# Performance work log

Hardware: AMD Instinct MI355X
Metric: run time of the kernel (lower is better)

The kernel has to match this reference:

```python
import jax, jax.numpy as jnp
import numpy as np

N = 50000   # full-order mesh size
n = 10      # latent dim
MU = 32     # neighbourhood / window size
B = 8       # batch of snapshots


def setup_inputs() -> dict:
    key = jax.random.key(0)
    ks = jax.random.split(key, 6)
    x = jax.random.normal(ks[0], (B, N), jnp.float32)
    enc_w = jax.random.normal(ks[1], (n, N), jnp.float32) * 0.01  # torch Linear weight [n, N]
    enc_b = jax.random.normal(ks[2], (n,), jnp.float32) * 0.01
    decoder = jax.random.uniform(ks[3], (n, N), jnp.float32, minval=-0.01, maxval=0.01)
    bandwidth_layers = jax.random.uniform(ks[4], (n, n, N), jnp.float32, minval=-0.01, maxval=0.01)
    neighbours = jax.random.randint(ks[5], (N, MU), 0, N, jnp.int32)
    return dict(x=x, enc_w=enc_w, enc_b=enc_b, decoder=decoder,
                bandwidth_layers=bandwidth_layers, neighbours=neighbours)


def reference(x, enc_w, enc_b, decoder, bandwidth_layers, neighbours):
    mu = neighbours.shape[1]
    # encode: torch Linear -> x @ W.T + b                      [B, n]
    encoded = x @ enc_w.T + enc_b
    # bandwidths: bmm(encoded.repeat(n,1,1), bw).permute(1,0,2) -> sigmoid   [B, n, N]
    w = jax.nn.sigmoid(jnp.einsum('bk,ikp->bip', encoded, bandwidth_layers))
    # bubble window per scalar w: relu(1 - x^2/(w*mu)^2), normalized over mu  [B, n, N, mu]
    xs2 = (jnp.arange(mu, dtype=x.dtype) ** 2)  # [mu]
    win = jax.nn.relu(1.0 - xs2 / (w[..., None] * mu) ** 2)
    win = win / jnp.sum(win, axis=-1, keepdims=True)
    # gather decoder rows at each node's neighbours            [n, N, mu]
    gathered = jnp.take(decoder, neighbours, axis=1)
    # smooth_vec: sum over neighbourhood                       [B, n, N]
    smoothed = jnp.einsum('ipm,bipm->bip', gathered, win)
    # final bmm: encoded [B,1,n] @ smoothed [B,n,N] -> [B,N]
    return jnp.einsum('bi,bip->bp', encoded, smoothed)
```

## Files before the change

kernel.cpp:

```cpp
#include <hip/hip_runtime.h>
#include <hip/hip_bf16.h>

#define N_NODES 50000
#define NLAT 10
#define MU 32
#define BATCH 8
#define CHUNK 2000
#define NCHUNK 25
#define ENC_BLOCKS (BATCH * NLAT * NCHUNK)
#define TR_BLOCKS ((N_NODES + 255) / 256)
#define DT_STRIDE 16
#define NPB 64
#define INV_STRIDE (NPB + 2)

__global__ __launch_bounds__(256) void encode_a_transpose(
    const float* __restrict__ x, const float* __restrict__ enc_w,
    const float* __restrict__ dec,
    float* __restrict__ partial, float* __restrict__ dec_t) {
    const int bid = blockIdx.x;
    if (bid < ENC_BLOCKS) {
        const int c  = bid % NCHUNK;
        const int bi = bid / NCHUNK;
        const int b = bi / NLAT, i = bi % NLAT;
        const float4* xr = (const float4*)(x + (size_t)b * N_NODES + c * CHUNK);
        const float4* wr = (const float4*)(enc_w + (size_t)i * N_NODES + c * CHUNK);
        float part = 0.0f;
        for (int q = threadIdx.x; q < CHUNK / 4; q += 256) {
            float4 xv = xr[q], wv = wr[q];
            part += xv.x * wv.x + xv.y * wv.y + xv.z * wv.z + xv.w * wv.w;
        }
        for (int off = 32; off; off >>= 1) part += __shfl_down(part, off, 64);
        __shared__ float s[4];
        if ((threadIdx.x & 63) == 0) s[threadIdx.x >> 6] = part;
        __syncthreads();
        if (threadIdx.x == 0) partial[bid] = (s[0] + s[1]) + (s[2] + s[3]);
    } else {
        const int p = (bid - ENC_BLOCKS) * 256 + threadIdx.x;
        if (p >= N_NODES) return;
        float v[DT_STRIDE];
        #pragma unroll
        for (int i = 0; i < NLAT; ++i) v[i] = dec[(size_t)i * N_NODES + p];
        #pragma unroll
        for (int i = NLAT; i < DT_STRIDE; ++i) v[i] = 0.0f;
        float4* dst = (float4*)(dec_t + (size_t)p * DT_STRIDE);
        #pragma unroll
        for (int q = 0; q < 4; ++q)
            dst[q] = make_float4(v[4*q], v[4*q+1], v[4*q+2], v[4*q+3]);
    }
}

__global__ __launch_bounds__(512) void nrbs_main_kernel(
    const float* __restrict__ dec_t,
    const float* __restrict__ bw,
    const int*   __restrict__ nbr,
    const float* __restrict__ partial,
    const float* __restrict__ enc_b,
    float*       __restrict__ out) {
    __shared__ float s_enc[BATCH * NLAT];
    __shared__ float s_inv[BATCH * NLAT * INV_STRIDE];
    __shared__ int   s_tm[NPB];
    const int tid = threadIdx.x;

    if (tid < BATCH * NLAT) {
        float s = 0.0f;
        #pragma unroll
        for (int c = 0; c < NCHUNK; ++c) s += partial[tid * NCHUNK + c];
        s_enc[tid] = s + enc_b[tid % NLAT];
    }
    if (tid < NPB) s_tm[tid] = 0;
    __syncthreads();

    {
        const int g    = tid >> 6;
        const int lane = tid & 63;
        const int p    = blockIdx.x * NPB + lane;
        if (p < N_NODES) {
            float tloc = 0.0f;
            for (int i = g; i < NLAT; i += 8) {
                float bwv[NLAT];
                #pragma unroll
                for (int k = 0; k < NLAT; ++k)
                    bwv[k] = bw[((size_t)(i * NLAT + k)) * N_NODES + p];
                #pragma unroll
                for (int b = 0; b < BATCH; ++b) {
                    float z = 0.0f;
                    #pragma unroll
                    for (int k = 0; k < NLAT; ++k)
                        z = fmaf(s_enc[b * NLAT + k], bwv[k], z);
                    const float w = 1.0f / (1.0f + __expf(-z));
                    const float t = w * (float)MU;
                    tloc = fmaxf(tloc, t);
                    s_inv[(b * NLAT + i) * INV_STRIDE + lane] = 1.0f / (t * t);
                }
            }
            atomicMax(&s_tm[lane], __float_as_int(tloc));
        }
    }
    __syncthreads();

    const int b  = tid & 7;
    const int nl = tid >> 3;
    const int p  = blockIdx.x * NPB + nl;
    if (p >= N_NODES) return;

    const int mcap = min(MU, (int)__int_as_float(s_tm[nl]) + 1);

    float inv[NLAT];
    #pragma unroll
    for (int i = 0; i < NLAT; ++i)
        inv[i] = s_inv[(b * NLAT + i) * INV_STRIDE + nl];

    float asum[NLAT], ssum[NLAT];
    #pragma unroll
    for (int i = 0; i < NLAT; ++i) { asum[i] = 0.0f; ssum[i] = 0.0f; }

    const int4* nb4 = (const int4*)(nbr + (size_t)p * MU);
    for (int q = 0; 4 * q < mcap; ++q) {
        const int4 v = nb4[q];
        const int idx[4] = {v.x, v.y, v.z, v.w};
        #pragma unroll
        for (int j = 0; j < 4; ++j) {
            const int m = 4 * q + j;
            const float m2 = (float)(m * m);
            const float4* gp = (const float4*)(dec_t + (size_t)idx[j] * DT_STRIDE);
            const float4 g0 = gp[0], g1 = gp[1];
            const float2 g2 = *(const float2*)(&gp[2]);
            const float g[NLAT] = {g0.x, g0.y, g0.z, g0.w,
                                   g1.x, g1.y, g1.z, g1.w, g2.x, g2.y};
            #pragma unroll
            for (int i = 0; i < NLAT; ++i) {
                const float win = fmaxf(0.0f, fmaf(-m2, inv[i], 1.0f));
                ssum[i] += win;
                asum[i] = fmaf(g[i], win, asum[i]);
            }
        }
    }

    float acc = 0.0f;
    #pragma unroll
    for (int i = 0; i < NLAT; ++i)
        acc = fmaf(s_enc[b * NLAT + i], asum[i] / ssum[i], acc);
    out[(size_t)b * N_NODES + p] = acc;
}

extern "C" void kernel_launch(void* const* d_in, const int* in_sizes, int n_in,
                              void* d_out, int out_size, void* d_ws, size_t ws_size,
                              hipStream_t stream) {
    const float* x       = (const float*)d_in[0];
    const float* enc_w   = (const float*)d_in[1];
    const float* enc_b   = (const float*)d_in[2];
    const float* decoder = (const float*)d_in[3];
    const float* bwl     = (const float*)d_in[4];
    const int*   nbr     = (const int*)d_in[5];
    float* out = (float*)d_out;

    float* partial = (float*)((char*)d_ws + 1024);
    float* dec_t   = (float*)((char*)d_ws + 65536);

    encode_a_transpose<<<ENC_BLOCKS + TR_BLOCKS, 256, 0, stream>>>(
        x, enc_w, decoder, partial, dec_t);

    const int blocks = (N_NODES + NPB - 1) / NPB;
    nrbs_main_kernel<<<blocks, 512, 0, stream>>>(
        dec_t, bwl, nbr, partial, enc_b, out);
}
```

Measured before the change: 110.7 us.

## Split main kernel work by latent pairs with packed float2 math and shared reduction

Restructures the main kernel so each of five wave groups owns two latent dimensions for all eight batches of a node, in place of one thread per (node, batch) covering all latents. Neighbour indices are staged in LDS, window accumulation uses packed two-wide FMA/max vectors, and per-latent contributions are reduced through shared memory before the output write. This cuts redundant dec_t gathers (each thread loads only two floats per neighbour) and uses packed FP32 math, at the cost of an extra shared-memory reduction pass, larger LDS use, and 320-thread blocks.

Measured after the change: 121.5 us. 1.1x slower.

```diff
diff --git a/kernel.cpp b/kernel.cpp
--- a/kernel.cpp
+++ b/kernel.cpp
@@ -11,7 +11,24 @@
 #define TR_BLOCKS ((N_NODES + 255) / 256)
 #define DT_STRIDE 16
 #define NPB 64
-#define INV_STRIDE (NPB + 2)
+
+typedef float v2f __attribute__((ext_vector_type(2)));
+
+static __device__ __forceinline__ v2f v2_fma(v2f a, v2f b, v2f c) {
+#if __has_builtin(__builtin_elementwise_fma)
+    return __builtin_elementwise_fma(a, b, c);
+#else
+    v2f r; r[0] = fmaf(a[0], b[0], c[0]); r[1] = fmaf(a[1], b[1], c[1]); return r;
+#endif
+}
+static __device__ __forceinline__ v2f v2_max0(v2f a) {
+#if __has_builtin(__builtin_elementwise_max)
+    v2f z = {0.0f, 0.0f};
+    return __builtin_elementwise_max(a, z);
+#else
+    v2f r; r[0] = fmaxf(a[0], 0.0f); r[1] = fmaxf(a[1], 0.0f); return r;
+#endif
+}
 
 __global__ __launch_bounds__(256) void encode_a_transpose(
     const float* __restrict__ x, const float* __restrict__ enc_w,
@@ -49,7 +66,7 @@
     }
 }
 
-__global__ __launch_bounds__(512) void nrbs_main_kernel(
+__global__ __launch_bounds__(320) void nrbs_main_kernel(
     const float* __restrict__ dec_t,
     const float* __restrict__ bw,
     const int*   __restrict__ nbr,
@@ -57,9 +74,12 @@
     const float* __restrict__ enc_b,
     float*       __restrict__ out) {
     __shared__ float s_enc[BATCH * NLAT];
-    __shared__ float s_inv[BATCH * NLAT * INV_STRIDE];
+    __shared__ float s_inv[NLAT][4][NPB][2];
+    __shared__ int   s_nbr[NPB][MU + 1];
     __shared__ int   s_tm[NPB];
-    const int tid = threadIdx.x;
+    __shared__ float s_red[NLAT][BATCH][NPB];
+    const int tid   = threadIdx.x;
+    const int node0 = blockIdx.x * NPB;
 
     if (tid < BATCH * NLAT) {
         float s = 0.0f;
@@ -68,79 +88,102 @@
         s_enc[tid] = s + enc_b[tid % NLAT];
     }
     if (tid < NPB) s_tm[tid] = 0;
+    for (int j = tid; j < NPB * MU / 4; j += 320) {
+        const int node = j >> 3, ch = j & 7;
+        int4 v = make_int4(0, 0, 0, 0);
+        if (node0 + node < N_NODES)
+            v = ((const int4*)(nbr + (size_t)(node0 + node) * MU))[ch];
+        s_nbr[node][ch * 4 + 0] = v.x; s_nbr[node][ch * 4 + 1] = v.y;
+        s_nbr[node][ch * 4 + 2] = v.z; s_nbr[node][ch * 4 + 3] = v.w;
+    }
     __syncthreads();
 
-    {
-        const int g    = tid >> 6;
-        const int lane = tid & 63;
-        const int p    = blockIdx.x * NPB + lane;
-        if (p < N_NODES) {
-            float tloc = 0.0f;
-            for (int i = g; i < NLAT; i += 8) {
-                float bwv[NLAT];
+    const int g  = tid >> 6;
+    const int nl = tid & 63;
+    const int i0 = 2 * g;
+    const int p  = node0 + nl;
+    const bool act = (p < N_NODES);
+
+    if (act) {
+        float tloc = 0.0f;
+        #pragma unroll
+        for (int ii = 0; ii < 2; ++ii) {
+            const int i = i0 + ii;
+            float bwv[NLAT];
+            #pragma unroll
+            for (int k = 0; k < NLAT; ++k)
+                bwv[k] = bw[((size_t)(i * NLAT + k)) * N_NODES + p];
+            #pragma unroll
+            for (int b = 0; b < BATCH; ++b) {
+                float z = 0.0f;
                 #pragma unroll
                 for (int k = 0; k < NLAT; ++k)
-                    bwv[k] = bw[((size_t)(i * NLAT + k)) * N_NODES + p];
-                #pragma unroll
-                for (int b = 0; b < BATCH; ++b) {
-                    float z = 0.0f;
-                    #pragma unroll
-                    for (int k = 0; k < NLAT; ++k)
-                        z = fmaf(s_enc[b * NLAT + k], bwv[k], z);
-                    const float w = 1.0f / (1.0f + __expf(-z));
-                    const float t = w * (float)MU;
-                    tloc = fmaxf(tloc, t);
-                    s_inv[(b * NLAT + i) * INV_STRIDE + lane] = 1.0f / (t * t);
+                    z = fmaf(s_enc[b * NLAT + k], bwv[k], z);
+                const float w = 1.0f / (1.0f + __expf(-z));
+                const float t = w * (float)MU;
+                tloc = fmaxf(tloc, t);
+                s_inv[i][b >> 1][nl][b & 1] = __builtin_amdgcn_rcpf(t * t);
+            }
+        }
+        atomicMax(&s_tm[nl], __float_as_int(tloc));
+    }
+    __syncthreads();
+
+    if (act) {
+        v2f inv2[2][4], asum[2][4], ssum[2][4];
+        #pragma unroll
+        for (int ii = 0; ii < 2; ++ii)
+            #pragma unroll
+            for (int b2 = 0; b2 < 4; ++b2) {
+                inv2[ii][b2] = *(const v2f*)&s_inv[i0 + ii][b2][nl][0];
+                asum[ii][b2] = (v2f){0.0f, 0.0f};
+                ssum[ii][b2] = (v2f){0.0f, 0.0f};
+            }
+        const int mcap = min(MU, (int)__int_as_float(s_tm[nl]) + 1);
+
+        for (int m = 0; m < mcap; ++m) {
+            const int idx = s_nbr[nl][m];
+            const v2f g2 = *(const v2f*)(dec_t + (size_t)idx * DT_STRIDE + i0);
+            const float m2 = (float)(m * m);
+            const v2f nm2 = {-m2, -m2}, one = {1.0f, 1.0f};
+            #pragma unroll
+            for (int ii = 0; ii < 2; ++ii) {
+                const v2f gb = {g2[ii], g2[ii]};
+                #pragma unroll
+                for (int b2 = 0; b2 < 4; ++b2) {
+                    v2f win = v2_max0(v2_fma(nm2, inv2[ii][b2], one));
+                    ssum[ii][b2] += win;
+                    asum[ii][b2] = v2_fma(gb, win, asum[ii][b2]);
                 }
             }
-            atomicMax(&s_tm[lane], __float_as_int(tloc));
-        }
+        }
+        #pragma unroll
+        for (int ii = 0; ii < 2; ++ii)
+            #pragma unroll
+            for (int b2 = 0; b2 < 4; ++b2)
+                #pragma unroll
+                for (int h = 0; h < 2; ++h) {
+                    const int b = b2 * 2 + h;
+                    s_red[i0 + ii][b][nl] =
+                        s_enc[b * NLAT + i0 + ii] * asum[ii][b2][h] *
+                        __builtin_amdgcn_rcpf(ssum[ii][b2][h]);
+                }
     }
     __syncthreads();
 
-    const int b  = tid & 7;
-    const int nl = tid >> 3;
-    const int p  = blockIdx.x * NPB + nl;
-    if (p >= N_NODES) return;
-
-    const int mcap = min(MU, (int)__int_as_float(s_tm[nl]) + 1);
-
-    float inv[NLAT];
-    #pragma unroll
-    for (int i = 0; i < NLAT; ++i)
-        inv[i] = s_inv[(b * NLAT + i) * INV_STRIDE + nl];
-
-    float asum[NLAT], ssum[NLAT];
-    #pragma unroll
-    for (int i = 0; i < NLAT; ++i) { asum[i] = 0.0f; ssum[i] = 0.0f; }
-
-    const int4* nb4 = (const int4*)(nbr + (size_t)p * MU);
-    for (int q = 0; 4 * q < mcap; ++q) {
-        const int4 v = nb4[q];
-        const int idx[4] = {v.x, v.y, v.z, v.w};
-        #pragma unroll
-        for (int j = 0; j < 4; ++j) {
-            const int m = 4 * q + j;
-            const float m2 = (float)(m * m);
-            const float4* gp = (const float4*)(dec_t + (size_t)idx[j] * DT_STRIDE);
-            const float4 g0 = gp[0], g1 = gp[1];
-            const float2 g2 = *(const float2*)(&gp[2]);
-            const float g[NLAT] = {g0.x, g0.y, g0.z, g0.w,
-                                   g1.x, g1.y, g1.z, g1.w, g2.x, g2.y};
-            #pragma unroll
-            for (int i = 0; i < NLAT; ++i) {
-                const float win = fmaxf(0.0f, fmaf(-m2, inv[i], 1.0f));
-                ssum[i] += win;
-                asum[i] = fmaf(g[i], win, asum[i]);
-            }
-        }
-    }
-
-    float acc = 0.0f;
-    #pragma unroll
-    for (int i = 0; i < NLAT; ++i)
-        acc = fmaf(s_enc[b * NLAT + i], asum[i] / ssum[i], acc);
-    out[(size_t)b * N_NODES + p] = acc;
+    if (tid < 256) {
+        const int b = tid >> 5, q = tid & 31;
+        #pragma unroll
+        for (int h = 0; h < 2; ++h) {
+            const int node = q + 32 * h, p2 = node0 + node;
+            if (p2 < N_NODES) {
+                float s = 0.0f;
+                #pragma unroll
+                for (int i = 0; i < NLAT; ++i) s += s_red[i][b][node];
+                out[(size_t)b * N_NODES + p2] = s;
+            }
+        }
+    }
 }
 
 extern "C" void kernel_launch(void* const* d_in, const int* in_sizes, int n_in,
@@ -161,6 +204,6 @@
         x, enc_w, decoder, partial, dec_t);
 
     const int blocks = (N_NODES + NPB - 1) / NPB;
-    nrbs_main_kernel<<<blocks, 512, 0, stream>>>(
+    nrbs_main_kernel<<<blocks, 320, 0, stream>>>(
         dec_t, bwl, nbr, partial, enc_b, out);
 }
```
